# Optimization experiments

Hardware: AMD Instinct MI355X
Metric: run time of the kernel (lower is better)

The kernel has to match this reference:

```python
import jax, jax.numpy as jnp
import numpy as np

B = 4          # batch
C_FEAT = 32    # shared feature channels
N_PARTS = 24   # body parts
H = 256        # triplane resolution (W = 3*H, three planes concatenated on width)
N_PTS = 8192   # sampled points per batch element
C = C_FEAT + N_PARTS


def setup_inputs() -> dict:
    key = jax.random.key(0)
    k1, k2 = jax.random.split(key)
    triplane = jax.random.normal(k1, (B, C, H, 3 * H), dtype=jnp.float32)
    # canonical coords in [-1, 1], one row per (point, part)
    triplane_coord_3d = jax.random.uniform(
        k2, (B * N_PTS * N_PARTS, 3), dtype=jnp.float32, minval=-1.0, maxval=1.0)
    index = jnp.arange(B * N_PTS, dtype=jnp.int32).reshape(B, N_PTS)
    return {"triplane": triplane, "triplane_coord_3d": triplane_coord_3d, "index": index}


def _bilinear(planes, uv):
    """planes: (B, 3, C, H, H); uv: (B, P, 3, 2) in [-1,1] (x->width, y->height).
    align_corners=False, border-clamped bilinear sample. Returns (B, P, 3, C)."""
    Hs = planes.shape[-1]
    px = (uv[..., 0] + 1.0) * (Hs * 0.5) - 0.5
    py = (uv[..., 1] + 1.0) * (Hs * 0.5) - 0.5
    x0f = jnp.floor(px)
    y0f = jnp.floor(py)
    wx = px - x0f
    wy = py - y0f
    x0 = jnp.clip(x0f.astype(jnp.int32), 0, Hs - 1)
    x1 = jnp.clip(x0f.astype(jnp.int32) + 1, 0, Hs - 1)
    y0 = jnp.clip(y0f.astype(jnp.int32), 0, Hs - 1)
    y1 = jnp.clip(y0f.astype(jnp.int32) + 1, 0, Hs - 1)
    bi = jnp.arange(planes.shape[0])[:, None, None]   # (B,1,1)
    ki = jnp.arange(3)[None, None, :]                 # (1,1,3)

    def g(yi, xi):
        return planes[bi, ki, :, yi, xi]              # (B, P, 3, C)

    return (g(y0, x0) * ((1 - wx) * (1 - wy))[..., None]
            + g(y0, x1) * (wx * (1 - wy))[..., None]
            + g(y1, x0) * ((1 - wx) * wy)[..., None]
            + g(y1, x1) * (wx * wy)[..., None])


def reference(triplane, triplane_coord_3d, index):
    Bq, n = index.shape
    # split width into the 3 concatenated planes -> (B, 3, C, H, H)
    planes = triplane.reshape(Bq, C, H, 3, H).transpose(0, 3, 1, 2, 4)
    # per-(point, part) coordinate rows
    rows = index[..., None] * N_PARTS + jnp.arange(N_PARTS, dtype=index.dtype)  # (B,n,P)
    xyz = triplane_coord_3d[rows]                                 # (B, n, P, 3)
    # plane uv: xy, xz, yz
    uv = jnp.stack([xyz[..., jnp.array([0, 1])],
                    xyz[..., jnp.array([0, 2])],
                    xyz[..., jnp.array([1, 2])]], axis=-2)        # (B, n, P, 3, 2)
    uv = uv.reshape(Bq, n * N_PARTS, 3, 2)
    samp = _bilinear(planes, uv).sum(axis=2)                      # sum over 3 planes -> (B, nP, C)
    samp = samp.reshape(Bq, n, N_PARTS, C)
    part_feature = samp[..., :C_FEAT].mean(axis=-1)               # (B, n, P)
    # part p's probability logit is channel 32+p sampled at part p's coords
    logits = samp[:, :, jnp.arange(N_PARTS), C_FEAT + jnp.arange(N_PARTS)]
    part_prob = jax.nn.softmax(logits, axis=-1)                   # (B, n, P)
    return (part_prob * part_feature).sum(axis=-1)                # (B, n)
```

## Files before the change

kernel.cpp:

```cpp
#include <hip/hip_runtime.h>

#define HS 256
#define W3 768
#define CCH 56
#define CF 32
#define NP 24
#define NPTS 8192
#define PLANE_SZ (HS * W3)

__global__ void tp_mean_kernel(const float* __restrict__ tri,
                               float* __restrict__ M) {
    int i4 = blockIdx.x * blockDim.x + threadIdx.x;
    int b = i4 / (PLANE_SZ / 4);
    int rem = i4 % (PLANE_SZ / 4);
    const float4* in = (const float4*)tri + (size_t)b * CCH * (PLANE_SZ / 4) + rem;
    float4 acc = {0.f, 0.f, 0.f, 0.f};
#pragma unroll
    for (int c = 0; c < CF; ++c) {
        float4 v = in[(size_t)c * (PLANE_SZ / 4)];
        acc.x += v.x; acc.y += v.y; acc.z += v.z; acc.w += v.w;
    }
    const float s = 1.0f / (float)CF;
    acc.x *= s; acc.y *= s; acc.z *= s; acc.w *= s;
    ((float4*)M)[(size_t)b * (PLANE_SZ / 4) + rem] = acc;
}

__device__ __forceinline__ void sample_row(const float* __restrict__ row,
                                           int x0, int x1,
                                           float& c0, float& c1) {
    const int xa = x0 & ~1;
    const float2 v = *reinterpret_cast<const float2*>(row + xa);
    if (x0 & 1) {
        c0 = v.y;
        c1 = (x1 == x0) ? v.y : row[x1];
    } else {
        c0 = v.x;
        c1 = (x1 == x0) ? v.x : v.y;
    }
}

__global__ __launch_bounds__(192) void tp_sample_kernel(
    const float* __restrict__ tri, const float* __restrict__ coords,
    const int* __restrict__ index, const float* __restrict__ M,
    float* __restrict__ out) {
    __shared__ float s_feat[NP][8];
    __shared__ float s_log[NP][8];

    const int tid = threadIdx.x;
    const int part = tid >> 3;
    const int lp = tid & 7;

    const int xcd = blockIdx.x & 7;
    const int slot = blockIdx.x >> 3;
    const int b = xcd >> 1;
    const int chunk = ((xcd & 1) << 9) + slot;
    const int point_base = b * NPTS + chunk * 8;
    const int point = point_base + lp;

    const int idx = index[point];
    const int row = idx * NP + part;
    const float x = coords[row * 3 + 0];
    const float y = coords[row * 3 + 1];
    const float z = coords[row * 3 + 2];

    const float us[3] = {x, x, y};
    const float vs[3] = {y, z, z};

    const float* __restrict__ Mb = M + (size_t)b * PLANE_SZ;
    const float* __restrict__ Tb = tri + (size_t)(b * CCH + CF + part) * PLANE_SZ;

    float feat = 0.f, lg = 0.f;
#pragma unroll
    for (int k = 0; k < 3; ++k) {
        const float px = (us[k] + 1.0f) * (HS * 0.5f) - 0.5f;
        const float py = (vs[k] + 1.0f) * (HS * 0.5f) - 0.5f;
        const float x0f = floorf(px);
        const float y0f = floorf(py);
        const float wx = px - x0f;
        const float wy = py - y0f;
        const int x0i = (int)x0f;
        const int y0i = (int)y0f;
        const int x0 = min(max(x0i, 0), HS - 1);
        const int x1 = min(max(x0i + 1, 0), HS - 1);
        const int y0 = min(max(y0i, 0), HS - 1);
        const int y1 = min(max(y0i + 1, 0), HS - 1);
        const float w00 = (1.f - wx) * (1.f - wy);
        const float w01 = wx * (1.f - wy);
        const float w10 = (1.f - wx) * wy;
        const float w11 = wx * wy;

        const int r0 = y0 * W3 + k * HS;
        const int r1 = y1 * W3 + k * HS;

        float m00, m01, m10, m11, t00, t01, t10, t11;
        sample_row(Mb + r0, x0, x1, m00, m01);
        sample_row(Mb + r1, x0, x1, m10, m11);
        sample_row(Tb + r0, x0, x1, t00, t01);
        sample_row(Tb + r1, x0, x1, t10, t11);

        feat += m00 * w00 + m01 * w01 + m10 * w10 + m11 * w11;
        lg   += t00 * w00 + t01 * w01 + t10 * w10 + t11 * w11;
    }

    s_feat[part][lp] = feat;
    s_log[part][lp] = lg;
    __syncthreads();

    if (tid < 8) {
        float mx = -1e30f;
#pragma unroll
        for (int j = 0; j < NP; ++j) mx = fmaxf(mx, s_log[j][tid]);
        float se = 0.f, acc = 0.f;
#pragma unroll
        for (int j = 0; j < NP; ++j) {
            const float e = __expf(s_log[j][tid] - mx);
            se += e;
            acc += e * s_feat[j][tid];
        }
        out[point_base + tid] = acc / se;
    }
}

extern "C" void kernel_launch(void* const* d_in, const int* in_sizes, int n_in,
                              void* d_out, int out_size, void* d_ws, size_t ws_size,
                              hipStream_t stream) {
    const float* tri = (const float*)d_in[0];
    const float* coords = (const float*)d_in[1];
    const int* index = (const int*)d_in[2];
    float* out = (float*)d_out;
    float* M = (float*)d_ws;

    tp_mean_kernel<<<(4 * PLANE_SZ / 4) / 256, 256, 0, stream>>>(tri, M);
    tp_sample_kernel<<<4096, 192, 0, stream>>>(tri, coords, index, M, out);
}
```

Baseline: 333.8 us.

## Split sampling into repack, part-major gather, and softmax kernels

Coordinates are first repacked into a part-major float4 array. A gather kernel then processes one (batch, part) pair per block, so each block reads a single logit channel plane, which should improve cache locality on the triplane. Per-part features and logits go to workspace buffers, and a separate softmax kernel reduces across parts. The cost is two extra launches plus extra global-memory round trips for the intermediate buffers.

```diff
diff --git a/kernel.cpp b/kernel.cpp
--- a/kernel.cpp
+++ b/kernel.cpp
@@ -6,6 +6,7 @@
 #define CF 32
 #define NP 24
 #define NPTS 8192
+#define NPOINTS (4 * NPTS)
 #define PLANE_SZ (HS * W3)
 
 __global__ void tp_mean_kernel(const float* __restrict__ tri,
@@ -25,6 +26,21 @@
     ((float4*)M)[(size_t)b * (PLANE_SZ / 4) + rem] = acc;
 }
 
+__global__ void tp_repack_kernel(const float* __restrict__ coords,
+                                 const int* __restrict__ index,
+                                 float4* __restrict__ Cp) {
+    int tid = blockIdx.x * blockDim.x + threadIdx.x;
+    int gpoint = tid / NP;
+    int part = tid - gpoint * NP;
+    int row = index[gpoint] * NP + part;
+    float4 v;
+    v.x = coords[row * 3 + 0];
+    v.y = coords[row * 3 + 1];
+    v.z = coords[row * 3 + 2];
+    v.w = 0.f;
+    Cp[(size_t)part * NPOINTS + gpoint] = v;
+}
+
 __device__ __forceinline__ void sample_row(const float* __restrict__ row,
                                            int x0, int x1,
                                            float& c0, float& c1) {
@@ -39,29 +55,20 @@
     }
 }
 
-__global__ __launch_bounds__(192) void tp_sample_kernel(
-    const float* __restrict__ tri, const float* __restrict__ coords,
-    const int* __restrict__ index, const float* __restrict__ M,
-    float* __restrict__ out) {
-    __shared__ float s_feat[NP][8];
-    __shared__ float s_log[NP][8];
+__global__ __launch_bounds__(256) void tp_gather_kernel(
+    const float* __restrict__ tri, const float4* __restrict__ Cp,
+    const float* __restrict__ M, float* __restrict__ wfeat,
+    float* __restrict__ wlog) {
+    const int w = (blockIdx.x & 7) * 384 + (blockIdx.x >> 3);
+    const int group = w >> 5;
+    const int chunk = w & 31;
+    const int b = group / NP;
+    const int part = group - b * NP;
 
-    const int tid = threadIdx.x;
-    const int part = tid >> 3;
-    const int lp = tid & 7;
+    const int gpoint = b * NPTS + chunk * 256 + threadIdx.x;
 
-    const int xcd = blockIdx.x & 7;
-    const int slot = blockIdx.x >> 3;
-    const int b = xcd >> 1;
-    const int chunk = ((xcd & 1) << 9) + slot;
-    const int point_base = b * NPTS + chunk * 8;
-    const int point = point_base + lp;
-
-    const int idx = index[point];
-    const int row = idx * NP + part;
-    const float x = coords[row * 3 + 0];
-    const float y = coords[row * 3 + 1];
-    const float z = coords[row * 3 + 2];
+    const float4 c4 = Cp[(size_t)part * NPOINTS + gpoint];
+    const float x = c4.x, y = c4.y, z = c4.z;
 
     const float us[3] = {x, x, y};
     const float vs[3] = {y, z, z};
@@ -102,23 +109,31 @@
         lg   += t00 * w00 + t01 * w01 + t10 * w10 + t11 * w11;
     }
 
-    s_feat[part][lp] = feat;
-    s_log[part][lp] = lg;
-    __syncthreads();
+    wfeat[(size_t)part * NPOINTS + gpoint] = feat;
+    wlog[(size_t)part * NPOINTS + gpoint] = lg;
+}
 
-    if (tid < 8) {
-        float mx = -1e30f;
+__global__ __launch_bounds__(256) void tp_softmax_kernel(
+    const float* __restrict__ wfeat, const float* __restrict__ wlog,
+    float* __restrict__ out) {
+    const int gpoint = blockIdx.x * 256 + threadIdx.x;
+    float f[NP], l[NP];
 #pragma unroll
-        for (int j = 0; j < NP; ++j) mx = fmaxf(mx, s_log[j][tid]);
-        float se = 0.f, acc = 0.f;
+    for (int p = 0; p < NP; ++p) {
+        f[p] = wfeat[(size_t)p * NPOINTS + gpoint];
+        l[p] = wlog[(size_t)p * NPOINTS + gpoint];
+    }
+    float mx = -1e30f;
 #pragma unroll
-        for (int j = 0; j < NP; ++j) {
-            const float e = __expf(s_log[j][tid] - mx);
-            se += e;
-            acc += e * s_feat[j][tid];
-        }
-        out[point_base + tid] = acc / se;
+    for (int p = 0; p < NP; ++p) mx = fmaxf(mx, l[p]);
+    float se = 0.f, acc = 0.f;
+#pragma unroll
+    for (int p = 0; p < NP; ++p) {
+        const float e = __expf(l[p] - mx);
+        se += e;
+        acc += e * f[p];
     }
+    out[gpoint] = acc / se;
 }
 
 extern "C" void kernel_launch(void* const* d_in, const int* in_sizes, int n_in,
@@ -128,8 +143,14 @@
     const float* coords = (const float*)d_in[1];
     const int* index = (const int*)d_in[2];
     float* out = (float*)d_out;
+
     float* M = (float*)d_ws;
+    float4* Cp = (float4*)(M + 4 * PLANE_SZ);
+    float* wfeat = (float*)(Cp + NP * NPOINTS);
+    float* wlog = wfeat + NP * NPOINTS;
 
     tp_mean_kernel<<<(4 * PLANE_SZ / 4) / 256, 256, 0, stream>>>(tri, M);
-    tp_sample_kernel<<<4096, 192, 0, stream>>>(tri, coords, index, M, out);
+    tp_repack_kernel<<<(NPOINTS * NP) / 256, 256, 0, stream>>>(coords, index, Cp);
+    tp_gather_kernel<<<3072, 256, 0, stream>>>(tri, Cp, M, wfeat, wlog);
+    tp_softmax_kernel<<<NPOINTS / 256, 256, 0, stream>>>(wfeat, wlog, out);
 }
```

New measurement: 326.5 us. -2.2%, faster.
